# Kernel optimization log

Hardware: AMD Instinct MI355X
Metric: run time of the kernel (lower is better)

## Reference

```python
import jax, jax.numpy as jnp
import numpy as np

N = 6144      # total nodes = num_data_qubits + num_checks
NQ = 3072     # num_data_qubits
D = 128       # hidden_dim
H = 4         # attention heads
C = D // H    # per-head channels (GATConv out_channels)
F_IN = 10     # node_feature_dim
L = 4         # num_gnn_layers
E = 393216    # num edges (before self-loops)


def _ln(x, g, b):
    m = x.mean(-1, keepdims=True)
    v = ((x - m) ** 2).mean(-1, keepdims=True)
    return (x - m) / jnp.sqrt(v + 1e-5) * g + b


def setup_inputs() -> dict:
    key = jax.random.key(0)
    ks = iter(jax.random.split(key, 64))

    def nrm(shape, scale):
        return jax.random.normal(next(ks), shape, jnp.float32) * scale

    inp = {}
    inp["node_features"] = nrm((N, F_IN), 1.0)
    inp["edge_index"] = jax.random.randint(next(ks), (2, E), 0, N, jnp.int32)
    inp["partner_encoding"] = nrm((N, D), 1.0)
    # node embedding MLP
    inp["emb_W"] = nrm((F_IN, D), F_IN ** -0.5)
    inp["emb_b"] = jnp.zeros((D,), jnp.float32)
    inp["emb_ln_g"] = jnp.ones((D,), jnp.float32)
    inp["emb_ln_b"] = jnp.zeros((D,), jnp.float32)
    # GAT layers (stacked over L)
    inp["gat_W"] = nrm((L, D, D), D ** -0.5)
    inp["gat_a_src"] = nrm((L, H, C), C ** -0.5)
    inp["gat_a_dst"] = nrm((L, H, C), C ** -0.5)
    inp["gat_b"] = jnp.zeros((L, D), jnp.float32)
    inp["ln_g"] = jnp.ones((L, D), jnp.float32)
    inp["ln_b"] = jnp.zeros((L, D), jnp.float32)
    # cross-panel multihead attention
    for nm in ["Wq", "Wk", "Wv", "Wo"]:
        inp[nm] = nrm((D, D), D ** -0.5)
    for nm in ["bq", "bk", "bv", "bo"]:
        inp[nm] = jnp.zeros((D,), jnp.float32)
    inp["ca_ln_g"] = jnp.ones((D,), jnp.float32)
    inp["ca_ln_b"] = jnp.zeros((D,), jnp.float32)
    # policy head
    inp["pW1"] = nrm((D, D), D ** -0.5); inp["pb1"] = jnp.zeros((D,), jnp.float32)
    inp["pW2"] = nrm((D, D // 2), D ** -0.5); inp["pb2"] = jnp.zeros((D // 2,), jnp.float32)
    inp["pW3"] = nrm((D // 2, 2), (D // 2) ** -0.5); inp["pb3"] = jnp.zeros((2,), jnp.float32)
    # value head
    inp["vW1"] = nrm((D, D), D ** -0.5); inp["vb1"] = jnp.zeros((D,), jnp.float32)
    inp["vW2"] = nrm((D, D // 2), D ** -0.5); inp["vb2"] = jnp.zeros((D // 2,), jnp.float32)
    inp["vW3"] = nrm((D // 2, 1), (D // 2) ** -0.5); inp["vb3"] = jnp.zeros((1,), jnp.float32)
    return inp


def reference(node_features, edge_index, partner_encoding,
              emb_W, emb_b, emb_ln_g, emb_ln_b,
              gat_W, gat_a_src, gat_a_dst, gat_b, ln_g, ln_b,
              Wq, bq, Wk, bk, Wv, bv, Wo, bo, ca_ln_g, ca_ln_b,
              pW1, pb1, pW2, pb2, pW3, pb3,
              vW1, vb1, vW2, vb2, vW3, vb3):
    # PyG GATConv default: add self-loops
    loops = jnp.arange(N, dtype=edge_index.dtype)
    src = jnp.concatenate([edge_index[0], loops])  # message source j
    dst = jnp.concatenate([edge_index[1], loops])  # aggregation target i

    x = jax.nn.relu(_ln(node_features @ emb_W + emb_b, emb_ln_g, emb_ln_b))

    for l in range(L):
        h = (x @ gat_W[l]).reshape(N, H, C)
        a_s = (h * gat_a_src[l]).sum(-1)  # [N,H]
        a_d = (h * gat_a_dst[l]).sum(-1)  # [N,H]
        e = jax.nn.leaky_relu(a_s[src] + a_d[dst], 0.2)  # [E+N,H]
        # segment softmax over edges sharing destination node
        mx = jax.ops.segment_max(e, dst, num_segments=N)
        ex = jnp.exp(e - mx[dst])
        denom = jax.ops.segment_sum(ex, dst, num_segments=N)
        alpha = ex / (denom[dst] + 1e-16)
        out = jax.ops.segment_sum(alpha[:, :, None] * h[src], dst, num_segments=N)
        out = out.reshape(N, D) + gat_b[l]
        x = _ln(x + jax.nn.relu(out), ln_g[l], ln_b[l])

    # cross-panel multihead attention (eval mode, batch of 1)
    q = (x @ Wq + bq).reshape(N, H, C)
    k = (partner_encoding @ Wk + bk).reshape(N, H, C)
    v = (partner_encoding @ Wv + bv).reshape(N, H, C)
    att = jax.nn.softmax(jnp.einsum('nhd,mhd->hnm', q, k) / np.float32(np.sqrt(C)), axis=-1)
    xa = jnp.einsum('hnm,mhd->nhd', att, v).reshape(N, D) @ Wo + bo
    x = _ln(x + xa, ca_ln_g, ca_ln_b)

    dq = x[:NQ]
    logits = jax.nn.relu(jax.nn.relu(dq @ pW1 + pb1) @ pW2 + pb2) @ pW3 + pb3
    pooled = x.mean(0, keepdims=True)
    value = jax.nn.relu(jax.nn.relu(pooled @ vW1 + vb1) @ vW2 + vb2) @ vW3 + vb3
    return logits, value, x
```

## Files before the change

### kernel.cpp

```cpp
#include <hip/hip_runtime.h>
#include <hip/hip_bf16.h>

#define N_NODES 6144
#define NQ_ 3072
#define D 128
#define H 4
#define C 32
#define F_IN 10
#define L_LAYERS 4
#define E_EDGES 393216
#define E_TOT (E_EDGES + N_NODES)
#define SPLITS 8
#define KV_PER (N_NODES / SPLITS)
#define NT_TOT (N_NODES / 32)
#define LOG2E 1.4426950408889634f

typedef __attribute__((ext_vector_type(8))) short bf16x8;
typedef __attribute__((ext_vector_type(4))) float f32x4;
typedef __attribute__((ext_vector_type(16))) float f32x16;

__device__ __forceinline__ unsigned short f2bf(float f) {
  unsigned u = __float_as_uint(f);
  unsigned r = (u + 0x7fffu + ((u >> 16) & 1u)) >> 16;
  return (unsigned short)r;
}

__device__ __forceinline__ float bf2f(unsigned short s) {
  return __uint_as_float(((unsigned)s) << 16);
}

__device__ __forceinline__ unsigned cvtpk(float lo, float hi) {
  unsigned r;
  asm volatile("v_cvt_pk_bf16_f32 %0, %1, %2" : "=v"(r) : "v"(lo), "v"(hi));
  return r;
}

#define P32SWAP(a, b) asm volatile("v_permlane32_swap_b32 %0, %1" : "+v"(a), "+v"(b))

#define MFMA32(A, B, CIN) __builtin_amdgcn_mfma_f32_32x32x16_bf16(A, B, CIN, 0, 0, 0)

__device__ __forceinline__ float red128_sum(float v, float* tmp2, int tid) {
#pragma unroll
  for (int m = 1; m < 64; m <<= 1) v += __shfl_xor(v, m, 64);
  __syncthreads();
  if ((tid & 63) == 0) tmp2[tid >> 6] = v;
  __syncthreads();
  return tmp2[0] + tmp2[1];
}

__device__ __forceinline__ f32x16 tile_gemm128(const unsigned short* __restrict__ A,
                                               const unsigned short* __restrict__ Bt,
                                               int row0, int col0, int qc, int hi) {
  const unsigned short* ap = A + (size_t)(row0 + qc) * 128 + hi * 8;
  const unsigned short* bp = Bt + (size_t)(col0 + qc) * 128 + hi * 8;
  f32x16 o = {0.f};
#pragma unroll
  for (int kk = 0; kk < 8; kk++) {
    bf16x8 a = *(const bf16x8*)(ap + kk * 16);
    bf16x8 b = *(const bf16x8*)(bp + kk * 16);
    o = MFMA32(a, b, o);
  }
  return o;
}

__global__ void k_zero(int* cnt, int* cur, float* pooled) {
  int i = blockIdx.x * blockDim.x + threadIdx.x;
  if (i < N_NODES) { cnt[i] = 0; cur[i] = 0; }
  if (i < D) pooled[i] = 0.f;
}

__global__ void k_hist(const int* __restrict__ dst, int* __restrict__ cnt) {
  for (int i = blockIdx.x * blockDim.x + threadIdx.x; i < E_EDGES; i += gridDim.x * blockDim.x)
    atomicAdd(&cnt[dst[i]], 1);
}

__global__ void k_scan(const int* __restrict__ cnt, int* __restrict__ indptr) {
  __shared__ int ps[256];
  int tid = threadIdx.x;
  const int CH = N_NODES / 256;
  int base = tid * CH;
  int loc[CH];
  int s = 0;
#pragma unroll
  for (int i = 0; i < CH; i++) { loc[i] = cnt[base + i] + 1; s += loc[i]; }
  ps[tid] = s;
  __syncthreads();
  for (int off = 1; off < 256; off <<= 1) {
    int v = (tid >= off) ? ps[tid - off] : 0;
    __syncthreads();
    ps[tid] += v;
    __syncthreads();
  }
  int run = (tid == 0) ? 0 : ps[tid - 1];
#pragma unroll
  for (int i = 0; i < CH; i++) { indptr[base + i] = run; run += loc[i]; }
  if (tid == 255) indptr[N_NODES] = run;
}

__global__ void k_scatter(const int* __restrict__ src, const int* __restrict__ dst,
                          const int* __restrict__ indptr, int* __restrict__ cur,
                          int* __restrict__ sorted) {
  for (int i = blockIdx.x * blockDim.x + threadIdx.x; i < E_TOT; i += gridDim.x * blockDim.x) {
    if (i < E_EDGES) {
      int d = dst[i];
      int p = atomicAdd(&cur[d], 1);
      sorted[indptr[d] + p] = src[i];
    } else {
      int n = i - E_EDGES;
      int p = atomicAdd(&cur[n], 1);
      sorted[indptr[n] + p] = n;
    }
  }
}

__global__ __launch_bounds__(128) void k_embed(const float* __restrict__ nf,
                                               const float* __restrict__ W,
                                               const float* __restrict__ b,
                                               const float* __restrict__ g,
                                               const float* __restrict__ bb,
                                               float* __restrict__ x,
                                               unsigned short* __restrict__ xbf) {
  int n = blockIdx.x, j = threadIdx.x;
  __shared__ float f[F_IN];
  __shared__ float tmp2[2];
  if (j < F_IN) f[j] = nf[n * F_IN + j];
  __syncthreads();
  float acc = b[j];
#pragma unroll
  for (int k = 0; k < F_IN; k++) acc += f[k] * W[k * D + j];
  float s1 = red128_sum(acc, tmp2, j);
  float s2 = red128_sum(acc * acc, tmp2, j);
  float mean = s1 * (1.f / D);
  float var = s2 * (1.f / D) - mean * mean;
  float y = (acc - mean) * rsqrtf(var + 1e-5f) * g[j] + bb[j];
  y = fmaxf(y, 0.f);
  x[n * D + j] = y;
  xbf[n * D + j] = f2bf(y);
}

__global__ void k_wprep(const float* __restrict__ W, unsigned short* __restrict__ wt) {
  int i = blockIdx.x * 256 + threadIdx.x;
  int l = i >> 14, rem = i & 16383, j = rem >> 7, k = rem & 127;
  wt[i] = f2bf(W[l * 16384 + k * 128 + j]);
}

__global__ void k_wqkvprep(const float* __restrict__ Wq, const float* __restrict__ Wk,
                           const float* __restrict__ Wv, const float* __restrict__ W1,
                           const float* __restrict__ W2, const float* __restrict__ Wo,
                           unsigned short* __restrict__ wqt, unsigned short* __restrict__ wkt,
                           unsigned short* __restrict__ wvt, unsigned short* __restrict__ w1t,
                           unsigned short* __restrict__ w2t, unsigned short* __restrict__ wot) {
  int i = blockIdx.x * 256 + threadIdx.x;
  if (i < 65536) {
    int m = i >> 14, loc = i & 16383, j = loc >> 7, k = loc & 127;
    const float* src = (m == 0) ? Wq : (m == 1) ? Wk : (m == 2) ? Wv : W1;
    unsigned short* dst = (m == 0) ? wqt : (m == 1) ? wkt : (m == 2) ? wvt : w1t;
    dst[loc] = f2bf(src[k * 128 + j]);
  } else if (i < 73728) {
    int loc = i - 65536, j = loc >> 7, k = loc & 127;
    w2t[loc] = f2bf(W2[k * 64 + j]);
  } else if (i < 90112) {
    int loc = i - 73728, j = loc >> 7, k = loc & 127;
    wot[loc] = f2bf(Wo[k * 128 + j]);
  }
}

__global__ void k_pebf(const float* __restrict__ pe, unsigned short* __restrict__ pebf) {
  int i = blockIdx.x * 256 + threadIdx.x;
  float4 v = *(const float4*)(pe + (size_t)i * 4);
  unsigned lo = (unsigned)f2bf(v.x) | ((unsigned)f2bf(v.y) << 16);
  unsigned hi = (unsigned)f2bf(v.z) | ((unsigned)f2bf(v.w) << 16);
  *(uint2*)(pebf + (size_t)i * 4) = make_uint2(lo, hi);
}

__global__ __launch_bounds__(256) void k_gat_gemm(const unsigned short* __restrict__ xbf,
                                                  const unsigned short* __restrict__ wt,
                                                  unsigned short* __restrict__ hbf) {
  int t = threadIdx.x;
  int w = t >> 6, l = t & 63, qc = l & 31, hi = l >> 5;
  int tile = blockIdx.x * 4 + w;
  int row0 = (tile >> 2) * 32, col0 = (tile & 3) * 32;
  f32x16 o = tile_gemm128(xbf, wt, row0, col0, qc, hi);
#pragma unroll
  for (int r = 0; r < 16; r++) {
    int rr = (r & 3) + 8 * (r >> 2) + 4 * hi;
    hbf[(size_t)(row0 + rr) * D + col0 + qc] = f2bf(o[r]);
  }
}

__global__ __launch_bounds__(128) void k_gat_attn(const unsigned short* __restrict__ hbf,
                                                  const float* __restrict__ asrc,
                                                  const float* __restrict__ adst,
                                                  float* __restrict__ a_s,
                                                  float* __restrict__ a_d) {
  int t = threadIdx.x;
  int ni = t >> 4, j = t & 15;
  int n = blockIdx.x * 8 + ni;
  const unsigned short* hp = hbf + (size_t)n * D + j * 8;
  float p = 0.f, q = 0.f;
#pragma unroll
  for (int c = 0; c < 8; c++) {
    float hv = bf2f(hp[c]);
    p += hv * asrc[j * 8 + c];
    q += hv * adst[j * 8 + c];
  }
  p += __shfl_xor(p, 1); p += __shfl_xor(p, 2);
  q += __shfl_xor(q, 1); q += __shfl_xor(q, 2);
  if ((j & 3) == 0) {
    int head = j >> 2;
    a_s[n * H + head] = p * LOG2E;
    a_d[n * H + head] = q * LOG2E;
  }
}

__device__ __forceinline__ float leaky(float v) { return v > 0.f ? v : 0.2f * v; }

__global__ __launch_bounds__(128) void k_gat_agg(const unsigned short* __restrict__ hbf,
                                                 const float* __restrict__ a_s,
                                                 const float* __restrict__ a_d,
                                                 const int* __restrict__ indptr,
                                                 const int* __restrict__ sorted,
                                                 const float* __restrict__ gb,
                                                 const float* __restrict__ g,
                                                 const float* __restrict__ bb,
                                                 float* __restrict__ x,
                                                 unsigned short* __restrict__ xbf) {
  int n = blockIdx.x, tid = threadIdx.x;
  int beg = indptr[n], end = indptr[n + 1];
  __shared__ int s_src[128];
  __shared__ float s_ex[128 * 4];
  __shared__ float tmp2[2];
  float4 ad = *(const float4*)&a_d[n * H];
  int hd = tid >> 5;
  float acc = 0.f;
  float d0 = 0.f, d1 = 0.f, d2 = 0.f, d3 = 0.f;

  for (int c0 = beg; c0 < end; c0 += 128) {
    __syncthreads();
    int e = c0 + tid;
    if (e < end) {
      int s = sorted[e];
      s_src[tid] = s;
      float4 as = *(const float4*)&a_s[s * H];
      float e0 = exp2f(leaky(as.x + ad.x));
      float e1 = exp2f(leaky(as.y + ad.y));
      float e2 = exp2f(leaky(as.z + ad.z));
      float e3 = exp2f(leaky(as.w + ad.w));
      s_ex[tid * 4 + 0] = e0;
      s_ex[tid * 4 + 1] = e1;
      s_ex[tid * 4 + 2] = e2;
      s_ex[tid * 4 + 3] = e3;
      d0 += e0; d1 += e1; d2 += e2; d3 += e3;
    }
    __syncthreads();
    int nc = min(128, end - c0);
#pragma unroll 4
    for (int i = 0; i < nc; i++) {
      acc += s_ex[i * 4 + hd] * bf2f(hbf[s_src[i] * D + tid]);
    }
  }
  float t0 = red128_sum(d0, tmp2, tid);
  float t1 = red128_sum(d1, tmp2, tid);
  float t2 = red128_sum(d2, tmp2, tid);
  float t3 = red128_sum(d3, tmp2, tid);
  float dd = (hd == 0) ? t0 : (hd == 1) ? t1 : (hd == 2) ? t2 : t3;
  float out = acc * (1.f / (dd + 1e-16f)) + gb[tid];
  float y = x[n * D + tid] + fmaxf(out, 0.f);
  float s1 = red128_sum(y, tmp2, tid);
  float s2 = red128_sum(y * y, tmp2, tid);
  float mean = s1 * (1.f / D);
  float var = s2 * (1.f / D) - mean * mean;
  float o = (y - mean) * rsqrtf(var + 1e-5f) * g[tid] + bb[tid];
  x[n * D + tid] = o;
  xbf[n * D + tid] = f2bf(o);
}

__global__ __launch_bounds__(256) void k_qkv_mfma(const unsigned short* __restrict__ xbf,
                                                  const unsigned short* __restrict__ pebf,
                                                  const unsigned short* __restrict__ wqt,
                                                  const unsigned short* __restrict__ wkt,
                                                  const unsigned short* __restrict__ wvt,
                                                  const float* __restrict__ bq,
                                                  const float* __restrict__ bk,
                                                  const float* __restrict__ bv,
                                                  unsigned short* __restrict__ qbf,
                                                  unsigned short* __restrict__ kpk,
                                                  unsigned short* __restrict__ vpk) {
  int t = threadIdx.x;
  int w = t >> 6, l = t & 63, qc = l & 31, hi = l >> 5;
  int m = blockIdx.y;
  int row0 = blockIdx.x * 32, col0 = w * 32;
  const unsigned short* A = (m == 0) ? xbf : pebf;
  const unsigned short* Bt = (m == 0) ? wqt : (m == 1) ? wkt : wvt;
  f32x16 o = tile_gemm128(A, Bt, row0, col0, qc, hi);
  int c = col0 + qc;
  int hh = col0 >> 5;
  int kt = row0 >> 5;
  if (m == 0) {
    const float sc = 0.25503491f;
    float bias = bq[c];
#pragma unroll
    for (int r = 0; r < 16; r++) {
      int rr = (r & 3) + 8 * (r >> 2) + 4 * hi;
      qbf[(size_t)(row0 + rr) * D + c] = f2bf((o[r] + bias) * sc);
    }
  } else if (m == 1) {
    float bias = bk[c];
    int kfrag = (qc >> 4) & 1, khi = (qc >> 3) & 1, kj = qc & 7;
    unsigned short* base = kpk + ((((size_t)hh * NT_TOT + kt) * 2 + kfrag) * 64 + khi * 32) * 8 + kj;
#pragma unroll
    for (int r = 0; r < 16; r++) {
      int rr = (r & 3) + 8 * (r >> 2) + 4 * hi;
      base[rr * 8] = f2bf(o[r] + bias);
    }
  } else {
    float bias = bv[c];
#pragma unroll
    for (int r = 0; r < 16; r++) {
      int rr = (r & 3) + 8 * (r >> 2) + 4 * hi;
      int vfrag = (rr >> 4) & 1, vhi = (rr >> 3) & 1, vj = rr & 7;
      vpk[((((size_t)hh * NT_TOT + kt) * 2 + vfrag) * 64 + vhi * 32 + qc) * 8 + vj] =
          f2bf(o[r] + bias);
    }
  }
}

#define ALOAD(KA0, KA1, VB0_, VB1_, TI) do { \
  const unsigned short* kp_ = kB + (size_t)(TI) * 1024 + l8; \
  const unsigned short* vp_ = vB + (size_t)(TI) * 1024 + l8; \
  KA0 = *(const bf16x8*)(kp_); \
  KA1 = *(const bf16x8*)(kp_ + 512); \
  VB0_ = *(const bf16x8*)(vp_); \
  VB1_ = *(const bf16x8*)(vp_ + 512); \
} while (0)

#define TILE32(KA0, KA1, VB0_, VB1_, O, LS) do { \
  f32x16 s = MFMA32(KA0, qa0, zz16); \
  s = MFMA32(KA1, qa1, s); \
  float p0 = __builtin_amdgcn_exp2f(s[0]), p1 = __builtin_amdgcn_exp2f(s[1]); \
  float p2 = __builtin_amdgcn_exp2f(s[2]), p3 = __builtin_amdgcn_exp2f(s[3]); \
  float p4 = __builtin_amdgcn_exp2f(s[4]), p5 = __builtin_amdgcn_exp2f(s[5]); \
  float p6 = __builtin_amdgcn_exp2f(s[6]), p7 = __builtin_amdgcn_exp2f(s[7]); \
  float p8 = __builtin_amdgcn_exp2f(s[8]), p9 = __builtin_amdgcn_exp2f(s[9]); \
  float pa = __builtin_amdgcn_exp2f(s[10]), pc = __builtin_amdgcn_exp2f(s[11]); \
  float pd = __builtin_amdgcn_exp2f(s[12]), pe_ = __builtin_amdgcn_exp2f(s[13]); \
  float pf = __builtin_amdgcn_exp2f(s[14]), pg = __builtin_amdgcn_exp2f(s[15]); \
  LS += (((p0 + p1) + (p2 + p3)) + ((p4 + p5) + (p6 + p7))) + \
        (((p8 + p9) + (pa + pc)) + ((pd + pe_) + (pf + pg))); \
  unsigned x0_ = cvtpk(p0, p1), x1_ = cvtpk(p2, p3); \
  unsigned y0_ = cvtpk(p4, p5), y1_ = cvtpk(p6, p7); \
  P32SWAP(x0_, y0_); P32SWAP(x1_, y1_); \
  unsigned x2_ = cvtpk(p8, p9), x3_ = cvtpk(pa, pc); \
  unsigned y2_ = cvtpk(pd, pe_), y3_ = cvtpk(pf, pg); \
  P32SWAP(x2_, y2_); P32SWAP(x3_, y3_); \
  union { unsigned u[4]; bf16x8 v; } fa_, fb_; \
  fa_.u[0] = x0_; fa_.u[1] = x1_; fa_.u[2] = y0_; fa_.u[3] = y1_; \
  fb_.u[0] = x2_; fb_.u[1] = x3_; fb_.u[2] = y2_; fb_.u[3] = y3_; \
  O = MFMA32(VB0_, fa_.v, O); \
  O = MFMA32(VB1_, fb_.v, O); \
} while (0)

__global__ __launch_bounds__(256) void k_attn_split(const unsigned short* __restrict__ qbf,
                                                    const unsigned short* __restrict__ kpk,
                                                    const unsigned short* __restrict__ vpk,
                                                    unsigned short* __restrict__ po,
                                                    float* __restrict__ pl) {
  int hh = blockIdx.y;
  int sp = blockIdx.z;
  int t = threadIdx.x;
  int wid = t >> 6, l = t & 63;
  int qc = l & 31, hi = l >> 5;
  int l8 = l * 8;
  int q0w = blockIdx.x * 128 + wid * 32;

  const f32x16 zz16 = {0.f};

  const unsigned short* qp = qbf + (size_t)(q0w + qc) * D + hh * 32 + hi * 8;
  bf16x8 qa0 = *(const bf16x8*)(qp);
  bf16x8 qa1 = *(const bf16x8*)(qp + 16);

  const unsigned short* kB = kpk + ((size_t)hh * NT_TOT + sp * (KV_PER / 32)) * 1024;
  const unsigned short* vB = vpk + ((size_t)hh * NT_TOT + sp * (KV_PER / 32)) * 1024;

  f32x16 oA = {0.f}, oB = {0.f};
  float lsA = 0.f, lsB = 0.f;

  bf16x8 ka0, ka1, va0, va1, kb0r, kb1r, vb0r, vb1r;
  ALOAD(ka0, ka1, va0, va1, 0);
  const int NT = KV_PER / 32;
  for (int it = 0; it < NT; it += 2) {
    ALOAD(kb0r, kb1r, vb0r, vb1r, it + 1);
    TILE32(ka0, ka1, va0, va1, oA, lsA);
    if (it + 2 < NT) ALOAD(ka0, ka1, va0, va1, it + 2);
    TILE32(kb0r, kb1r, vb0r, vb1r, oB, lsB);
  }

  f32x16 o = oA + oB;
  float lsum = lsA + lsB;
  float lt = lsum + __shfl_xor(lsum, 32, 64);
  size_t pbase = (size_t)(sp * H + hh) * N_NODES + q0w + qc;
  unsigned short* pop = po + pbase * 32 + 4 * hi;
  uint2 v0, v1, v2, v3;
  v0.x = cvtpk(o[0], o[1]);   v0.y = cvtpk(o[2], o[3]);
  v1.x = cvtpk(o[4], o[5]);   v1.y = cvtpk(o[6], o[7]);
  v2.x = cvtpk(o[8], o[9]);   v2.y = cvtpk(o[10], o[11]);
  v3.x = cvtpk(o[12], o[13]); v3.y = cvtpk(o[14], o[15]);
  *(uint2*)(pop)      = v0;
  *(uint2*)(pop + 8)  = v1;
  *(uint2*)(pop + 16) = v2;
  *(uint2*)(pop + 24) = v3;
  if (l < 32) {
    pl[pbase] = lt;
  }
}

__global__ __launch_bounds__(256) void k_attn_combine(const unsigned short* __restrict__ po,
                                                      const float* __restrict__ pl,
                                                      unsigned short* __restrict__ xabf) {
  int t = blockIdx.x * 256 + threadIdx.x;
  int q = t >> 6, cp = t & 63;
  int c2 = cp * 2, hh = c2 >> 5, c = c2 & 31;
  int base = hh * N_NODES + q;
  const int SN = H * N_NODES;
  float ll = 0.f, olo = 0.f, ohi = 0.f;
#pragma unroll
  for (int s = 0; s < SPLITS; s++) {
    ll += pl[s * SN + base];
    unsigned dw = *(const unsigned*)(po + ((size_t)(s * SN + base)) * 32 + c);
    olo += bf2f((unsigned short)(dw & 0xffff));
    ohi += bf2f((unsigned short)(dw >> 16));
  }
  float inv = 1.f / ll;
  *(unsigned*)(xabf + (size_t)q * D + c2) = cvtpk(olo * inv, ohi * inv);
}

__global__ __launch_bounds__(256) void k_ca_gemm(const unsigned short* __restrict__ xabf,
                                                 const unsigned short* __restrict__ wot,
                                                 const float* __restrict__ bo,
                                                 float* __restrict__ yb) {
  int t = threadIdx.x;
  int w = t >> 6, l = t & 63, qc = l & 31, hi = l >> 5;
  int row0 = blockIdx.x * 32, col0 = w * 32;
  f32x16 o = tile_gemm128(xabf, wot, row0, col0, qc, hi);
  float bias = bo[col0 + qc];
#pragma unroll
  for (int r = 0; r < 16; r++) {
    int rr = (r & 3) + 8 * (r >> 2) + 4 * hi;
    yb[(size_t)(row0 + rr) * D + col0 + qc] = o[r] + bias;
  }
}

__global__ __launch_bounds__(128) void k_ca_ln(const float* __restrict__ yb,
                                               const float* __restrict__ g,
                                               const float* __restrict__ bb,
                                               float* __restrict__ x,
                                               unsigned short* __restrict__ xbf,
                                               float* __restrict__ pooled,
                                               float* __restrict__ outx) {
  int tid = threadIdx.x, r0 = blockIdx.x * 8;
  __shared__ float tmp2[2];
  float gv = g[tid], bv = bb[tid];
  float psum = 0.f;
#pragma unroll
  for (int r = 0; r < 8; r++) {
    int n = r0 + r;
    float y = x[n * D + tid] + yb[n * D + tid];
    float t1 = red128_sum(y, tmp2, tid);
    float t2 = red128_sum(y * y, tmp2, tid);
    float mean = t1 * (1.f / D);
    float var = t2 * (1.f / D) - mean * mean;
    float o = (y - mean) * rsqrtf(var + 1e-5f) * gv + bv;
    x[n * D + tid] = o;
    xbf[n * D + tid] = f2bf(o);
    outx[n * D + tid] = o;
    psum += o;
  }
  atomicAdd(&pooled[tid], psum);
}

__global__ __launch_bounds__(256) void k_policy1(const unsigned short* __restrict__ xbf,
                                                 const unsigned short* __restrict__ w1t,
                                                 const float* __restrict__ b1,
                                                 unsigned short* __restrict__ h1) {
  int t = threadIdx.x;
  int w = t >> 6, l = t & 63, qc = l & 31, hi = l >> 5;
  int row0 = blockIdx.x * 32, col0 = w * 32;
  f32x16 o = tile_gemm128(xbf, w1t, row0, col0, qc, hi);
  float bias = b1[col0 + qc];
#pragma unroll
  for (int r = 0; r < 16; r++) {
    int rr = (r & 3) + 8 * (r >> 2) + 4 * hi;
    h1[(size_t)(row0 + rr) * D + col0 + qc] = f2bf(fmaxf(o[r] + bias, 0.f));
  }
}

__global__ __launch_bounds__(128) void k_policy2(const unsigned short* __restrict__ h1,
                                                 const unsigned short* __restrict__ w2t,
                                                 const float* __restrict__ b2,
                                                 unsigned short* __restrict__ h2) {
  int t = threadIdx.x;
  int w = t >> 6, l = t & 63, qc = l & 31, hi = l >> 5;
  int row0 = blockIdx.x * 32, col0 = w * 32;
  f32x16 o = tile_gemm128(h1, w2t, row0, col0, qc, hi);
  float bias = b2[col0 + qc];
#pragma unroll
  for (int r = 0; r < 16; r++) {
    int rr = (r & 3) + 8 * (r >> 2) + 4 * hi;
    h2[(size_t)(row0 + rr) * 64 + col0 + qc] = f2bf(fmaxf(o[r] + bias, 0.f));
  }
}

__global__ __launch_bounds__(256) void k_policy3(const unsigned short* __restrict__ h2,
                                                 const float* __restrict__ W3,
                                                 const float* __restrict__ b3,
                                                 float* __restrict__ logits) {
  int t = threadIdx.x;
  int wv = t >> 6, l = t & 63;
  int n = blockIdx.x * 4 + wv;
  float h = bf2f(h2[(size_t)n * 64 + l]);
  float p0 = h * W3[l * 2];
  float p1 = h * W3[l * 2 + 1];
#pragma unroll
  for (int m = 1; m < 64; m <<= 1) { p0 += __shfl_xor(p0, m, 64); p1 += __shfl_xor(p1, m, 64); }
  if (l == 0) {
    logits[n * 2] = p0 + b3[0];
    logits[n * 2 + 1] = p1 + b3[1];
  }
}

__global__ __launch_bounds__(128) void k_value(const float* __restrict__ pooled,
                                               const float* __restrict__ W1,
                                               const float* __restrict__ b1,
                                               const float* __restrict__ W2,
                                               const float* __restrict__ b2,
                                               const float* __restrict__ W3,
                                               const float* __restrict__ b3,
                                               float* __restrict__ val) {
  int tid = threadIdx.x;
  __shared__ float ps[D], v1[D], v2[64];
  ps[tid] = pooled[tid] * (1.f / N_NODES);
  __syncthreads();
  float a = b1[tid];
  for (int kk = 0; kk < D; kk++) a += ps[kk] * W1[kk * D + tid];
  v1[tid] = fmaxf(a, 0.f);
  __syncthreads();
  if (tid < 64) {
    float a2 = b2[tid];
    for (int kk = 0; kk < D; kk++) a2 += v1[kk] * W2[kk * 64 + tid];
    v2[tid] = fmaxf(a2, 0.f);
  }
  __syncthreads();
  float p = (tid < 64) ? v2[tid] * W3[tid] : 0.f;
#pragma unroll
  for (int m = 1; m < 64; m <<= 1) p += __shfl_xor(p, m, 64);
  if (tid == 0) val[0] = p + b3[0];
}

extern "C" void kernel_launch(void* const* d_in, const int* in_sizes, int n_in,
                              void* d_out, int out_size, void* d_ws, size_t ws_size,
                              hipStream_t stream) {
  const float* nf   = (const float*)d_in[0];
  const int*   ei   = (const int*)d_in[1];
  const float* pe   = (const float*)d_in[2];
  const float* embW = (const float*)d_in[3];
  const float* embB = (const float*)d_in[4];
  const float* elng = (const float*)d_in[5];
  const float* elnb = (const float*)d_in[6];
  const float* gatW = (const float*)d_in[7];
  const float* aS   = (const float*)d_in[8];
  const float* aD   = (const float*)d_in[9];
  const float* gatB = (const float*)d_in[10];
  const float* lng  = (const float*)d_in[11];
  const float* lnb  = (const float*)d_in[12];
  const float* Wq   = (const float*)d_in[13];
  const float* Wk   = (const float*)d_in[14];
  const float* Wv   = (const float*)d_in[15];
  const float* Wo   = (const float*)d_in[16];
  const float* bq   = (const float*)d_in[17];
  const float* bk   = (const float*)d_in[18];
  const float* bv   = (const float*)d_in[19];
  const float* bo   = (const float*)d_in[20];
  const float* cag  = (const float*)d_in[21];
  const float* cab  = (const float*)d_in[22];
  const float* pW1  = (const float*)d_in[23];
  const float* pb1  = (const float*)d_in[24];
  const float* pW2  = (const float*)d_in[25];
  const float* pb2  = (const float*)d_in[26];
  const float* pW3  = (const float*)d_in[27];
  const float* pb3  = (const float*)d_in[28];
  const float* vW1  = (const float*)d_in[29];
  const float* vb1  = (const float*)d_in[30];
  const float* vW2  = (const float*)d_in[31];
  const float* vb2  = (const float*)d_in[32];
  const float* vW3  = (const float*)d_in[33];
  const float* vb3  = (const float*)d_in[34];

  float* fw = (float*)d_ws;
  float* x      = fw; fw += N_NODES * D;
  float* hbuf   = fw; fw += N_NODES * D;
  float* a_s    = fw; fw += N_NODES * H;
  float* a_d    = fw; fw += N_NODES * H;
  float* pooled = fw; fw += 128;
  float* pl     = fw; fw += SPLITS * H * N_NODES;
  unsigned short* ub = (unsigned short*)fw;
  unsigned short* po   = ub; ub += (size_t)SPLITS * H * N_NODES * 32;
  unsigned short* qbf  = ub; ub += N_NODES * D;
  unsigned short* kpk  = ub; ub += N_NODES * D;
  unsigned short* vpk  = ub; ub += N_NODES * D;
  unsigned short* xbf  = ub; ub += N_NODES * D;
  unsigned short* pebf = ub; ub += N_NODES * D;
  unsigned short* wtb  = ub; ub += L_LAYERS * D * D;
  unsigned short* wqt  = ub; ub += D * D;
  unsigned short* wkt  = ub; ub += D * D;
  unsigned short* wvt  = ub; ub += D * D;
  unsigned short* w1t  = ub; ub += D * D;
  unsigned short* w2t  = ub; ub += 64 * D;
  unsigned short* wot  = ub; ub += D * D;
  int* ib     = (int*)ub;
  int* cnt    = ib; ib += N_NODES;
  int* cur    = ib; ib += N_NODES;
  int* indptr = ib; ib += N_NODES + 16;
  int* sorted = ib;

  unsigned short* hbf  = (unsigned short*)hbuf;
  float* yb            = hbuf;
  unsigned short* xabf = kpk;
  unsigned short* h1   = qbf;
  unsigned short* h2   = qbf + (size_t)NQ_ * D;

  float* out    = (float*)d_out;
  float* logits = out;
  float* val    = out + NQ_ * 2;
  float* outx   = out + NQ_ * 2 + 1;

  const int* esrc = ei;
  const int* edst = ei + E_EDGES;

  hipLaunchKernelGGL(k_zero, dim3(24), dim3(256), 0, stream, cnt, cur, pooled);
  hipLaunchKernelGGL(k_hist, dim3(512), dim3(256), 0, stream, edst, cnt);
  hipLaunchKernelGGL(k_scan, dim3(1), dim3(256), 0, stream, cnt, indptr);
  hipLaunchKernelGGL(k_scatter, dim3(512), dim3(256), 0, stream, esrc, edst, indptr, cur, sorted);
  hipLaunchKernelGGL(k_embed, dim3(N_NODES), dim3(128), 0, stream, nf, embW, embB, elng, elnb, x, xbf);
  hipLaunchKernelGGL(k_wprep, dim3(L_LAYERS * D * D / 256), dim3(256), 0, stream, gatW, wtb);
  hipLaunchKernelGGL(k_wqkvprep, dim3(352), dim3(256), 0, stream,
                     Wq, Wk, Wv, pW1, pW2, Wo, wqt, wkt, wvt, w1t, w2t, wot);
  hipLaunchKernelGGL(k_pebf, dim3(N_NODES * D / 1024), dim3(256), 0, stream, pe, pebf);
  for (int l = 0; l < L_LAYERS; l++) {
    hipLaunchKernelGGL(k_gat_gemm, dim3(N_NODES / 32), dim3(256), 0, stream,
                       xbf, wtb + l * D * D, hbf);
    hipLaunchKernelGGL(k_gat_attn, dim3(N_NODES / 8), dim3(128), 0, stream,
                       hbf, aS + l * D, aD + l * D, a_s, a_d);
    hipLaunchKernelGGL(k_gat_agg, dim3(N_NODES), dim3(128), 0, stream,
                       hbf, a_s, a_d, indptr, sorted, gatB + l * D, lng + l * D, lnb + l * D, x, xbf);
  }
  hipLaunchKernelGGL(k_qkv_mfma, dim3(N_NODES / 32, 3), dim3(256), 0, stream,
                     xbf, pebf, wqt, wkt, wvt, bq, bk, bv, qbf, kpk, vpk);
  hipLaunchKernelGGL(k_attn_split, dim3(N_NODES / 128, H, SPLITS), dim3(256), 0, stream,
                     qbf, kpk, vpk, po, pl);
  hipLaunchKernelGGL(k_attn_combine, dim3(N_NODES * D / 512), dim3(256), 0, stream,
                     po, pl, xabf);
  hipLaunchKernelGGL(k_ca_gemm, dim3(N_NODES / 32), dim3(256), 0, stream, xabf, wot, bo, yb);
  hipLaunchKernelGGL(k_ca_ln, dim3(N_NODES / 8), dim3(128), 0, stream,
                     yb, cag, cab, x, xbf, pooled, outx);
  hipLaunchKernelGGL(k_policy1, dim3(NQ_ / 32), dim3(256), 0, stream, xbf, w1t, pb1, h1);
  hipLaunchKernelGGL(k_policy2, dim3(NQ_ / 32), dim3(128), 0, stream, h1, w2t, pb2, h2);
  hipLaunchKernelGGL(k_policy3, dim3(NQ_ / 4), dim3(256), 0, stream, h2, pW3, pb3, logits);
  hipLaunchKernelGGL(k_value, dim3(1), dim3(128), 0, stream,
                     pooled, vW1, vb1, vW2, vb2, vW3, vb3, val);
}
```

Baseline: 273.9 us.

## Split GAT aggregation edges across four waves with packed bf16 loads

The GAT aggregation kernel now runs 256 threads per node. Each of four wavefronts handles every fourth edge, and each lane loads two bf16 channels with one 32-bit read. The partial sums from the waves are reduced through shared memory, and the softmax denominator and LayerNorm reductions are fused into fewer barrier rounds. Separately, the embed and cross-attention LayerNorm kernels compute sum and sum-of-squares together in one reduction. The goal is more memory-level parallelism on the irregular gathers and fewer syncthreads, at the cost of more shared memory and idle threads in the epilogue.

```diff
diff --git a/kernel.cpp b/kernel.cpp
--- a/kernel.cpp
+++ b/kernel.cpp
@@ -48,6 +48,22 @@
   return tmp2[0] + tmp2[1];
 }
 
+__device__ __forceinline__ void red128_sum2(float& a, float& b, float* tmp4, int tid) {
+#pragma unroll
+  for (int m = 1; m < 64; m <<= 1) {
+    a += __shfl_xor(a, m, 64);
+    b += __shfl_xor(b, m, 64);
+  }
+  __syncthreads();
+  if ((tid & 63) == 0) {
+    tmp4[(tid >> 6) * 2]     = a;
+    tmp4[(tid >> 6) * 2 + 1] = b;
+  }
+  __syncthreads();
+  a = tmp4[0] + tmp4[2];
+  b = tmp4[1] + tmp4[3];
+}
+
 __device__ __forceinline__ f32x16 tile_gemm128(const unsigned short* __restrict__ A,
                                                const unsigned short* __restrict__ Bt,
                                                int row0, int col0, int qc, int hi) {
@@ -122,14 +138,14 @@
                                                unsigned short* __restrict__ xbf) {
   int n = blockIdx.x, j = threadIdx.x;
   __shared__ float f[F_IN];
-  __shared__ float tmp2[2];
+  __shared__ float tmp4[4];
   if (j < F_IN) f[j] = nf[n * F_IN + j];
   __syncthreads();
   float acc = b[j];
 #pragma unroll
   for (int k = 0; k < F_IN; k++) acc += f[k] * W[k * D + j];
-  float s1 = red128_sum(acc, tmp2, j);
-  float s2 = red128_sum(acc * acc, tmp2, j);
+  float s1 = acc, s2 = acc * acc;
+  red128_sum2(s1, s2, tmp4, j);
   float mean = s1 * (1.f / D);
   float var = s2 * (1.f / D) - mean * mean;
   float y = (acc - mean) * rsqrtf(var + 1e-5f) * g[j] + bb[j];
@@ -215,7 +231,7 @@
 
 __device__ __forceinline__ float leaky(float v) { return v > 0.f ? v : 0.2f * v; }
 
-__global__ __launch_bounds__(128) void k_gat_agg(const unsigned short* __restrict__ hbf,
+__global__ __launch_bounds__(256) void k_gat_agg(const unsigned short* __restrict__ hbf,
                                                  const float* __restrict__ a_s,
                                                  const float* __restrict__ a_d,
                                                  const int* __restrict__ indptr,
@@ -226,16 +242,19 @@
                                                  float* __restrict__ x,
                                                  unsigned short* __restrict__ xbf) {
   int n = blockIdx.x, tid = threadIdx.x;
+  int wv = tid >> 6, l = tid & 63;
   int beg = indptr[n], end = indptr[n + 1];
-  __shared__ int s_src[128];
-  __shared__ float s_ex[128 * 4];
-  __shared__ float tmp2[2];
+  __shared__ int s_src[256];
+  __shared__ float s_ex[256 * 4];
+  __shared__ float2 red2[4][64];
+  __shared__ float rtmp[16];
+  __shared__ float tmp8[8];
   float4 ad = *(const float4*)&a_d[n * H];
-  int hd = tid >> 5;
-  float acc = 0.f;
+  int hsel = l >> 4;
+  float accx = 0.f, accy = 0.f;
   float d0 = 0.f, d1 = 0.f, d2 = 0.f, d3 = 0.f;
 
-  for (int c0 = beg; c0 < end; c0 += 128) {
+  for (int c0 = beg; c0 < end; c0 += 256) {
     __syncthreads();
     int e = c0 + tid;
     if (e < end) {
@@ -253,26 +272,61 @@
       d0 += e0; d1 += e1; d2 += e2; d3 += e3;
     }
     __syncthreads();
-    int nc = min(128, end - c0);
+    int nc = min(256, end - c0);
 #pragma unroll 4
-    for (int i = 0; i < nc; i++) {
-      acc += s_ex[i * 4 + hd] * bf2f(hbf[s_src[i] * D + tid]);
+    for (int i = wv; i < nc; i += 4) {
+      float al = s_ex[i * 4 + hsel];
+      int s = s_src[i];
+      unsigned dw = *(const unsigned*)(hbf + (size_t)s * D + l * 2);
+      accx += al * bf2f((unsigned short)(dw & 0xffff));
+      accy += al * bf2f((unsigned short)(dw >> 16));
     }
   }
-  float t0 = red128_sum(d0, tmp2, tid);
-  float t1 = red128_sum(d1, tmp2, tid);
-  float t2 = red128_sum(d2, tmp2, tid);
-  float t3 = red128_sum(d3, tmp2, tid);
-  float dd = (hd == 0) ? t0 : (hd == 1) ? t1 : (hd == 2) ? t2 : t3;
-  float out = acc * (1.f / (dd + 1e-16f)) + gb[tid];
-  float y = x[n * D + tid] + fmaxf(out, 0.f);
-  float s1 = red128_sum(y, tmp2, tid);
-  float s2 = red128_sum(y * y, tmp2, tid);
-  float mean = s1 * (1.f / D);
-  float var = s2 * (1.f / D) - mean * mean;
-  float o = (y - mean) * rsqrtf(var + 1e-5f) * g[tid] + bb[tid];
-  x[n * D + tid] = o;
-  xbf[n * D + tid] = f2bf(o);
+  red2[wv][l] = make_float2(accx, accy);
+#pragma unroll
+  for (int m = 1; m < 64; m <<= 1) {
+    d0 += __shfl_xor(d0, m, 64);
+    d1 += __shfl_xor(d1, m, 64);
+    d2 += __shfl_xor(d2, m, 64);
+    d3 += __shfl_xor(d3, m, 64);
+  }
+  if (l == 0) {
+    rtmp[wv * 4 + 0] = d0; rtmp[wv * 4 + 1] = d1;
+    rtmp[wv * 4 + 2] = d2; rtmp[wv * 4 + 3] = d3;
+  }
+  __syncthreads();
+
+  float y = 0.f;
+  int c = tid;
+  if (tid < 128) {
+    const float* rp0 = (const float*)&red2[0][c >> 1];
+    const float* rp1 = (const float*)&red2[1][c >> 1];
+    const float* rp2 = (const float*)&red2[2][c >> 1];
+    const float* rp3 = (const float*)&red2[3][c >> 1];
+    int par = c & 1;
+    float sum = rp0[par] + rp1[par] + rp2[par] + rp3[par];
+    int hd = c >> 5;
+    float dd = rtmp[hd] + rtmp[4 + hd] + rtmp[8 + hd] + rtmp[12 + hd];
+    float outv = sum * (1.f / (dd + 1e-16f)) + gb[c];
+    y = x[n * D + c] + fmaxf(outv, 0.f);
+  }
+  float sy = y, syy = y * y;
+#pragma unroll
+  for (int m = 1; m < 64; m <<= 1) {
+    sy += __shfl_xor(sy, m, 64);
+    syy += __shfl_xor(syy, m, 64);
+  }
+  if (l == 0) { tmp8[wv * 2] = sy; tmp8[wv * 2 + 1] = syy; }
+  __syncthreads();
+  if (tid < 128) {
+    float s1 = tmp8[0] + tmp8[2] + tmp8[4] + tmp8[6];
+    float s2 = tmp8[1] + tmp8[3] + tmp8[5] + tmp8[7];
+    float mean = s1 * (1.f / D);
+    float var = s2 * (1.f / D) - mean * mean;
+    float o = (y - mean) * rsqrtf(var + 1e-5f) * g[c] + bb[c];
+    x[n * D + c] = o;
+    xbf[n * D + c] = f2bf(o);
+  }
 }
 
 __global__ __launch_bounds__(256) void k_qkv_mfma(const unsigned short* __restrict__ xbf,
@@ -458,17 +512,17 @@
                                                float* __restrict__ pooled,
                                                float* __restrict__ outx) {
   int tid = threadIdx.x, r0 = blockIdx.x * 8;
-  __shared__ float tmp2[2];
+  __shared__ float tmp4[4];
   float gv = g[tid], bv = bb[tid];
   float psum = 0.f;
 #pragma unroll
   for (int r = 0; r < 8; r++) {
     int n = r0 + r;
     float y = x[n * D + tid] + yb[n * D + tid];
-    float t1 = red128_sum(y, tmp2, tid);
-    float t2 = red128_sum(y * y, tmp2, tid);
-    float mean = t1 * (1.f / D);
-    float var = t2 * (1.f / D) - mean * mean;
+    float s1 = y, s2 = y * y;
+    red128_sum2(s1, s2, tmp4, tid);
+    float mean = s1 * (1.f / D);
+    float var = s2 * (1.f / D) - mean * mean;
     float o = (y - mean) * rsqrtf(var + 1e-5f) * gv + bv;
     x[n * D + tid] = o;
     xbf[n * D + tid] = f2bf(o);
@@ -650,7 +704,7 @@
                        xbf, wtb + l * D * D, hbf);
     hipLaunchKernelGGL(k_gat_attn, dim3(N_NODES / 8), dim3(128), 0, stream,
                        hbf, aS + l * D, aD + l * D, a_s, a_d);
-    hipLaunchKernelGGL(k_gat_agg, dim3(N_NODES), dim3(128), 0, stream,
+    hipLaunchKernelGGL(k_gat_agg, dim3(N_NODES), dim3(256), 0, stream,
                        hbf, a_s, a_d, indptr, sorted, gatB + l * D, lng + l * D, lnb + l * D, x, xbf);
   }
   hipLaunchKernelGGL(k_qkv_mfma, dim3(N_NODES / 32, 3), dim3(256), 0, stream,
```

Result: no change. 268.7 us (-1.9%).

## Split GAT edge softmax into edge kernel and wave-per-node aggregation; merge prep kernels

Applied to the files above, without the earlier changes.

Merges the zeroing, weight-conversion and partner-encoding conversion kernels into one launch. Adds a destination array in the CSR scatter so a new per-edge kernel can compute exponentiated attention scores into a global buffer. The aggregation kernel is rewritten to one wavefront per node with two channels per lane, which drops shared-memory staging and block barriers in favour of wave shuffles. It also vectorizes the attention-logit kernel and fuses paired LayerNorm reductions. The cost is an extra kernel launch per layer and a large edge-score buffer that must be written and read back.

```diff
diff --git a/kernel.cpp b/kernel.cpp
--- a/kernel.cpp
+++ b/kernel.cpp
@@ -39,13 +39,20 @@
 
 #define MFMA32(A, B, CIN) __builtin_amdgcn_mfma_f32_32x32x16_bf16(A, B, CIN, 0, 0, 0)
 
-__device__ __forceinline__ float red128_sum(float v, float* tmp2, int tid) {
-#pragma unroll
-  for (int m = 1; m < 64; m <<= 1) v += __shfl_xor(v, m, 64);
+__device__ __forceinline__ void red128_sum2(float& a, float& b, float* tmp4, int tid) {
+#pragma unroll
+  for (int m = 1; m < 64; m <<= 1) {
+    a += __shfl_xor(a, m, 64);
+    b += __shfl_xor(b, m, 64);
+  }
   __syncthreads();
-  if ((tid & 63) == 0) tmp2[tid >> 6] = v;
+  if ((tid & 63) == 0) {
+    tmp4[(tid >> 6) * 2]     = a;
+    tmp4[(tid >> 6) * 2 + 1] = b;
+  }
   __syncthreads();
-  return tmp2[0] + tmp2[1];
+  a = tmp4[0] + tmp4[2];
+  b = tmp4[1] + tmp4[3];
 }
 
 __device__ __forceinline__ f32x16 tile_gemm128(const unsigned short* __restrict__ A,
@@ -63,11 +70,52 @@
   return o;
 }
 
-__global__ void k_zero(int* cnt, int* cur, float* pooled) {
-  int i = blockIdx.x * blockDim.x + threadIdx.x;
-  if (i < N_NODES) { cnt[i] = 0; cur[i] = 0; }
-  if (i < D) pooled[i] = 0.f;
-}
+__global__ void k_prep(int* cnt, int* cur, float* pooled,
+                       const float* __restrict__ gatW, unsigned short* __restrict__ wt,
+                       const float* __restrict__ Wq, const float* __restrict__ Wk,
+                       const float* __restrict__ Wv, const float* __restrict__ W1,
+                       const float* __restrict__ W2, const float* __restrict__ Wo,
+                       unsigned short* __restrict__ wqt, unsigned short* __restrict__ wkt,
+                       unsigned short* __restrict__ wvt, unsigned short* __restrict__ w1t,
+                       unsigned short* __restrict__ w2t, unsigned short* __restrict__ wot,
+                       const float* __restrict__ pe, unsigned short* __restrict__ pebf) {
+  int i = blockIdx.x * 256 + threadIdx.x;
+  if (i < 6272) {
+    if (i < N_NODES) { cnt[i] = 0; cur[i] = 0; }
+    else pooled[i - N_NODES] = 0.f;
+    return;
+  }
+  i -= 6272;
+  if (i < 65536) {
+    int l = i >> 14, rem = i & 16383, j = rem >> 7, k = rem & 127;
+    wt[i] = f2bf(gatW[l * 16384 + k * 128 + j]);
+    return;
+  }
+  i -= 65536;
+  if (i < 90112) {
+    if (i < 65536) {
+      int m = i >> 14, loc = i & 16383, j = loc >> 7, k = loc & 127;
+      const float* src = (m == 0) ? Wq : (m == 1) ? Wk : (m == 2) ? Wv : W1;
+      unsigned short* dst = (m == 0) ? wqt : (m == 1) ? wkt : (m == 2) ? wvt : w1t;
+      dst[loc] = f2bf(src[k * 128 + j]);
+    } else if (i < 73728) {
+      int loc = i - 65536, j = loc >> 7, k = loc & 127;
+      w2t[loc] = f2bf(W2[k * 64 + j]);
+    } else {
+      int loc = i - 73728, j = loc >> 7, k = loc & 127;
+      wot[loc] = f2bf(Wo[k * 128 + j]);
+    }
+    return;
+  }
+  i -= 90112;
+  if (i < N_NODES * D / 4) {
+    float4 v = ((const float4*)pe)[i];
+    unsigned lo = (unsigned)f2bf(v.x) | ((unsigned)f2bf(v.y) << 16);
+    unsigned hi = (unsigned)f2bf(v.z) | ((unsigned)f2bf(v.w) << 16);
+    *(uint2*)(pebf + (size_t)i * 4) = make_uint2(lo, hi);
+  }
+}
+#define PREP_ITEMS (6272 + 65536 + 90112 + N_NODES * D / 4)
 
 __global__ void k_hist(const int* __restrict__ dst, int* __restrict__ cnt) {
   for (int i = blockIdx.x * blockDim.x + threadIdx.x; i < E_EDGES; i += gridDim.x * blockDim.x)
@@ -99,16 +147,20 @@
 
 __global__ void k_scatter(const int* __restrict__ src, const int* __restrict__ dst,
                           const int* __restrict__ indptr, int* __restrict__ cur,
-                          int* __restrict__ sorted) {
+                          int* __restrict__ sorted, int* __restrict__ dpos) {
   for (int i = blockIdx.x * blockDim.x + threadIdx.x; i < E_TOT; i += gridDim.x * blockDim.x) {
     if (i < E_EDGES) {
       int d = dst[i];
       int p = atomicAdd(&cur[d], 1);
-      sorted[indptr[d] + p] = src[i];
+      int pos = indptr[d] + p;
+      sorted[pos] = src[i];
+      dpos[pos] = d;
     } else {
       int n = i - E_EDGES;
       int p = atomicAdd(&cur[n], 1);
-      sorted[indptr[n] + p] = n;
+      int pos = indptr[n] + p;
+      sorted[pos] = n;
+      dpos[pos] = n;
     }
   }
 }
@@ -122,14 +174,14 @@
                                                unsigned short* __restrict__ xbf) {
   int n = blockIdx.x, j = threadIdx.x;
   __shared__ float f[F_IN];
-  __shared__ float tmp2[2];
+  __shared__ float tmp4[4];
   if (j < F_IN) f[j] = nf[n * F_IN + j];
   __syncthreads();
   float acc = b[j];
 #pragma unroll
   for (int k = 0; k < F_IN; k++) acc += f[k] * W[k * D + j];
-  float s1 = red128_sum(acc, tmp2, j);
-  float s2 = red128_sum(acc * acc, tmp2, j);
+  float s1 = acc, s2 = acc * acc;
+  red128_sum2(s1, s2, tmp4, j);
   float mean = s1 * (1.f / D);
   float var = s2 * (1.f / D) - mean * mean;
   float y = (acc - mean) * rsqrtf(var + 1e-5f) * g[j] + bb[j];
@@ -138,41 +190,6 @@
   xbf[n * D + j] = f2bf(y);
 }
 
-__global__ void k_wprep(const float* __restrict__ W, unsigned short* __restrict__ wt) {
-  int i = blockIdx.x * 256 + threadIdx.x;
-  int l = i >> 14, rem = i & 16383, j = rem >> 7, k = rem & 127;
-  wt[i] = f2bf(W[l * 16384 + k * 128 + j]);
-}
-
-__global__ void k_wqkvprep(const float* __restrict__ Wq, const float* __restrict__ Wk,
-                           const float* __restrict__ Wv, const float* __restrict__ W1,
-                           const float* __restrict__ W2, const float* __restrict__ Wo,
-                           unsigned short* __restrict__ wqt, unsigned short* __restrict__ wkt,
-                           unsigned short* __restrict__ wvt, unsigned short* __restrict__ w1t,
-                           unsigned short* __restrict__ w2t, unsigned short* __restrict__ wot) {
-  int i = blockIdx.x * 256 + threadIdx.x;
-  if (i < 65536) {
-    int m = i >> 14, loc = i & 16383, j = loc >> 7, k = loc & 127;
-    const float* src = (m == 0) ? Wq : (m == 1) ? Wk : (m == 2) ? Wv : W1;
-    unsigned short* dst = (m == 0) ? wqt : (m == 1) ? wkt : (m == 2) ? wvt : w1t;
-    dst[loc] = f2bf(src[k * 128 + j]);
-  } else if (i < 73728) {
-    int loc = i - 65536, j = loc >> 7, k = loc & 127;
-    w2t[loc] = f2bf(W2[k * 64 + j]);
-  } else if (i < 90112) {
-    int loc = i - 73728, j = loc >> 7, k = loc & 127;
-    wot[loc] = f2bf(Wo[k * 128 + j]);
-  }
-}
-
-__global__ void k_pebf(const float* __restrict__ pe, unsigned short* __restrict__ pebf) {
-  int i = blockIdx.x * 256 + threadIdx.x;
-  float4 v = *(const float4*)(pe + (size_t)i * 4);
-  unsigned lo = (unsigned)f2bf(v.x) | ((unsigned)f2bf(v.y) << 16);
-  unsigned hi = (unsigned)f2bf(v.z) | ((unsigned)f2bf(v.w) << 16);
-  *(uint2*)(pebf + (size_t)i * 4) = make_uint2(lo, hi);
-}
-
 __global__ __launch_bounds__(256) void k_gat_gemm(const unsigned short* __restrict__ xbf,
                                                   const unsigned short* __restrict__ wt,
                                                   unsigned short* __restrict__ hbf) {
@@ -196,14 +213,17 @@
   int t = threadIdx.x;
   int ni = t >> 4, j = t & 15;
   int n = blockIdx.x * 8 + ni;
-  const unsigned short* hp = hbf + (size_t)n * D + j * 8;
-  float p = 0.f, q = 0.f;
-#pragma unroll
-  for (int c = 0; c < 8; c++) {
-    float hv = bf2f(hp[c]);
-    p += hv * asrc[j * 8 + c];
-    q += hv * adst[j * 8 + c];
-  }
+  bf16x8 hv = *(const bf16x8*)(hbf + (size_t)n * D + j * 8);
+  float4 a0 = *(const float4*)(asrc + j * 8);
+  float4 a1 = *(const float4*)(asrc + j * 8 + 4);
+  float4 d0 = *(const float4*)(adst + j * 8);
+  float4 d1 = *(const float4*)(adst + j * 8 + 4);
+  float h0 = bf2f(hv[0]), h1 = bf2f(hv[1]), h2 = bf2f(hv[2]), h3 = bf2f(hv[3]);
+  float h4 = bf2f(hv[4]), h5 = bf2f(hv[5]), h6 = bf2f(hv[6]), h7 = bf2f(hv[7]);
+  float p = h0 * a0.x + h1 * a0.y + h2 * a0.z + h3 * a0.w +
+            h4 * a1.x + h5 * a1.y + h6 * a1.z + h7 * a1.w;
+  float q = h0 * d0.x + h1 * d0.y + h2 * d0.z + h3 * d0.w +
+            h4 * d1.x + h5 * d1.y + h6 * d1.z + h7 * d1.w;
   p += __shfl_xor(p, 1); p += __shfl_xor(p, 2);
   q += __shfl_xor(q, 1); q += __shfl_xor(q, 2);
   if ((j & 3) == 0) {
@@ -215,9 +235,26 @@
 
 __device__ __forceinline__ float leaky(float v) { return v > 0.f ? v : 0.2f * v; }
 
-__global__ __launch_bounds__(128) void k_gat_agg(const unsigned short* __restrict__ hbf,
+__global__ __launch_bounds__(256) void k_edge_ex(const int* __restrict__ sorted,
+                                                 const int* __restrict__ dpos,
                                                  const float* __restrict__ a_s,
                                                  const float* __restrict__ a_d,
+                                                 float4* __restrict__ ex) {
+  int i = blockIdx.x * 256 + threadIdx.x;
+  if (i >= E_TOT) return;
+  int s = sorted[i], d = dpos[i];
+  float4 as = *(const float4*)(a_s + s * 4);
+  float4 ad = *(const float4*)(a_d + d * 4);
+  float4 r;
+  r.x = exp2f(leaky(as.x + ad.x));
+  r.y = exp2f(leaky(as.y + ad.y));
+  r.z = exp2f(leaky(as.z + ad.z));
+  r.w = exp2f(leaky(as.w + ad.w));
+  ex[i] = r;
+}
+
+__global__ __launch_bounds__(256) void k_gat_agg(const unsigned short* __restrict__ hbf,
+                                                 const float4* __restrict__ ex,
                                                  const int* __restrict__ indptr,
                                                  const int* __restrict__ sorted,
                                                  const float* __restrict__ gb,
@@ -225,54 +262,42 @@
                                                  const float* __restrict__ bb,
                                                  float* __restrict__ x,
                                                  unsigned short* __restrict__ xbf) {
-  int n = blockIdx.x, tid = threadIdx.x;
+  int tid = threadIdx.x, wv = tid >> 6, l = tid & 63;
+  int n = blockIdx.x * 4 + wv;
   int beg = indptr[n], end = indptr[n + 1];
-  __shared__ int s_src[128];
-  __shared__ float s_ex[128 * 4];
-  __shared__ float tmp2[2];
-  float4 ad = *(const float4*)&a_d[n * H];
-  int hd = tid >> 5;
-  float acc = 0.f;
-  float d0 = 0.f, d1 = 0.f, d2 = 0.f, d3 = 0.f;
-
-  for (int c0 = beg; c0 < end; c0 += 128) {
-    __syncthreads();
-    int e = c0 + tid;
-    if (e < end) {
-      int s = sorted[e];
-      s_src[tid] = s;
-      float4 as = *(const float4*)&a_s[s * H];
-      float e0 = exp2f(leaky(as.x + ad.x));
-      float e1 = exp2f(leaky(as.y + ad.y));
-      float e2 = exp2f(leaky(as.z + ad.z));
-      float e3 = exp2f(leaky(as.w + ad.w));
-      s_ex[tid * 4 + 0] = e0;
-      s_ex[tid * 4 + 1] = e1;
-      s_ex[tid * 4 + 2] = e2;
-      s_ex[tid * 4 + 3] = e3;
-      d0 += e0; d1 += e1; d2 += e2; d3 += e3;
-    }
-    __syncthreads();
-    int nc = min(128, end - c0);
+  int hsel = l >> 4;
+  int c = l * 2;
+  const unsigned short* hb = hbf + c;
+  float accx = 0.f, accy = 0.f, dsum = 0.f;
 #pragma unroll 4
-    for (int i = 0; i < nc; i++) {
-      acc += s_ex[i * 4 + hd] * bf2f(hbf[s_src[i] * D + tid]);
-    }
-  }
-  float t0 = red128_sum(d0, tmp2, tid);
-  float t1 = red128_sum(d1, tmp2, tid);
-  float t2 = red128_sum(d2, tmp2, tid);
-  float t3 = red128_sum(d3, tmp2, tid);
-  float dd = (hd == 0) ? t0 : (hd == 1) ? t1 : (hd == 2) ? t2 : t3;
-  float out = acc * (1.f / (dd + 1e-16f)) + gb[tid];
-  float y = x[n * D + tid] + fmaxf(out, 0.f);
-  float s1 = red128_sum(y, tmp2, tid);
-  float s2 = red128_sum(y * y, tmp2, tid);
-  float mean = s1 * (1.f / D);
-  float var = s2 * (1.f / D) - mean * mean;
-  float o = (y - mean) * rsqrtf(var + 1e-5f) * g[tid] + bb[tid];
-  x[n * D + tid] = o;
-  xbf[n * D + tid] = f2bf(o);
+  for (int e = beg; e < end; e++) {
+    float4 e4 = ex[e];
+    float al = (hsel < 2) ? ((hsel == 0) ? e4.x : e4.y) : ((hsel == 2) ? e4.z : e4.w);
+    int s = sorted[e];
+    unsigned dw = *(const unsigned*)(hb + (size_t)s * D);
+    accx = fmaf(al, bf2f((unsigned short)(dw & 0xffff)), accx);
+    accy = fmaf(al, bf2f((unsigned short)(dw >> 16)), accy);
+    dsum += al;
+  }
+  float inv = 1.f / (dsum + 1e-16f);
+  float o0 = accx * inv + gb[c];
+  float o1 = accy * inv + gb[c + 1];
+  float2 xv = *(const float2*)(x + (size_t)n * D + c);
+  float y0 = xv.x + fmaxf(o0, 0.f);
+  float y1 = xv.y + fmaxf(o1, 0.f);
+  float sy = y0 + y1, syy = y0 * y0 + y1 * y1;
+#pragma unroll
+  for (int m = 1; m < 64; m <<= 1) {
+    sy += __shfl_xor(sy, m, 64);
+    syy += __shfl_xor(syy, m, 64);
+  }
+  float mean = sy * (1.f / D);
+  float var = syy * (1.f / D) - mean * mean;
+  float rs = rsqrtf(var + 1e-5f);
+  float r0 = (y0 - mean) * rs * g[c] + bb[c];
+  float r1 = (y1 - mean) * rs * g[c + 1] + bb[c + 1];
+  *(float2*)(x + (size_t)n * D + c) = make_float2(r0, r1);
+  *(unsigned*)(xbf + (size_t)n * D + c) = cvtpk(r0, r1);
 }
 
 __global__ __launch_bounds__(256) void k_qkv_mfma(const unsigned short* __restrict__ xbf,
@@ -458,17 +483,17 @@
                                                float* __restrict__ pooled,
                                                float* __restrict__ outx) {
   int tid = threadIdx.x, r0 = blockIdx.x * 8;
-  __shared__ float tmp2[2];
+  __shared__ float tmp4[4];
   float gv = g[tid], bv = bb[tid];
   float psum = 0.f;
 #pragma unroll
   for (int r = 0; r < 8; r++) {
     int n = r0 + r;
     float y = x[n * D + tid] + yb[n * D + tid];
-    float t1 = red128_sum(y, tmp2, tid);
-    float t2 = red128_sum(y * y, tmp2, tid);
-    float mean = t1 * (1.f / D);
-    float var = t2 * (1.f / D) - mean * mean;
+    float s1 = y, s2 = y * y;
+    red128_sum2(s1, s2, tmp4, tid);
+    float mean = s1 * (1.f / D);
+    float var = s2 * (1.f / D) - mean * mean;
     float o = (y - mean) * rsqrtf(var + 1e-5f) * gv + bv;
     x[n * D + tid] = o;
     xbf[n * D + tid] = f2bf(o);
@@ -602,6 +627,7 @@
   float* a_d    = fw; fw += N_NODES * H;
   float* pooled = fw; fw += 128;
   float* pl     = fw; fw += SPLITS * H * N_NODES;
+  float* exbuf  = fw; fw += (size_t)E_TOT * 4;
   unsigned short* ub = (unsigned short*)fw;
   unsigned short* po   = ub; ub += (size_t)SPLITS * H * N_NODES * 32;
   unsigned short* qbf  = ub; ub += N_NODES * D;
@@ -620,7 +646,8 @@
   int* cnt    = ib; ib += N_NODES;
   int* cur    = ib; ib += N_NODES;
   int* indptr = ib; ib += N_NODES + 16;
-  int* sorted = ib;
+  int* sorted = ib; ib += E_TOT;
+  int* dpos   = ib;
 
   unsigned short* hbf  = (unsigned short*)hbuf;
   float* yb            = hbuf;
@@ -636,22 +663,24 @@
   const int* esrc = ei;
   const int* edst = ei + E_EDGES;
 
-  hipLaunchKernelGGL(k_zero, dim3(24), dim3(256), 0, stream, cnt, cur, pooled);
+  hipLaunchKernelGGL(k_prep, dim3((PREP_ITEMS + 255) / 256), dim3(256), 0, stream,
+                     cnt, cur, pooled, gatW, wtb, Wq, Wk, Wv, pW1, pW2, Wo,
+                     wqt, wkt, wvt, w1t, w2t, wot, pe, pebf);
   hipLaunchKernelGGL(k_hist, dim3(512), dim3(256), 0, stream, edst, cnt);
   hipLaunchKernelGGL(k_scan, dim3(1), dim3(256), 0, stream, cnt, indptr);
-  hipLaunchKernelGGL(k_scatter, dim3(512), dim3(256), 0, stream, esrc, edst, indptr, cur, sorted);
+  hipLaunchKernelGGL(k_scatter, dim3(512), dim3(256), 0, stream, esrc, edst, indptr, cur,
+                     sorted, dpos);
   hipLaunchKernelGGL(k_embed, dim3(N_NODES), dim3(128), 0, stream, nf, embW, embB, elng, elnb, x, xbf);
-  hipLaunchKernelGGL(k_wprep, dim3(L_LAYERS * D * D / 256), dim3(256), 0, stream, gatW, wtb);
-  hipLaunchKernelGGL(k_wqkvprep, dim3(352), dim3(256), 0, stream,
-                     Wq, Wk, Wv, pW1, pW2, Wo, wqt, wkt, wvt, w1t, w2t, wot);
-  hipLaunchKernelGGL(k_pebf, dim3(N_NODES * D / 1024), dim3(256), 0, stream, pe, pebf);
   for (int l = 0; l < L_LAYERS; l++) {
     hipLaunchKernelGGL(k_gat_gemm, dim3(N_NODES / 32), dim3(256), 0, stream,
                        xbf, wtb + l * D * D, hbf);
     hipLaunchKernelGGL(k_gat_attn, dim3(N_NODES / 8), dim3(128), 0, stream,
                        hbf, aS + l * D, aD + l * D, a_s, a_d);
-    hipLaunchKernelGGL(k_gat_agg, dim3(N_NODES), dim3(128), 0, stream,
-                       hbf, a_s, a_d, indptr, sorted, gatB + l * D, lng + l * D, lnb + l * D, x, xbf);
+    hipLaunchKernelGGL(k_edge_ex, dim3((E_TOT + 255) / 256), dim3(256), 0, stream,
+                       sorted, dpos, a_s, a_d, (float4*)exbuf);
+    hipLaunchKernelGGL(k_gat_agg, dim3(N_NODES / 4), dim3(256), 0, stream,
+                       hbf, (const float4*)exbuf, indptr, sorted,
+                       gatB + l * D, lng + l * D, lnb + l * D, x, xbf);
   }
   hipLaunchKernelGGL(k_qkv_mfma, dim3(N_NODES / 32, 3), dim3(256), 0, stream,
                      xbf, pebf, wqt, wkt, wvt, bq, bk, bv, qbf, kpk, vpk);
```

Result: slower. 436.8 us (+59.5%).
